# Kernel tuning notes

Measured on AMD Instinct MI355X. Metric: run time of the kernel, lower is better.

The kernel has to match this reference:

```python
import jax, jax.numpy as jnp
import numpy as np

NUM_ELEC = 128
TIME_STEPS = 128  # must equal NUM_ELEC for the original module's matmuls to be shape-consistent
NUM_VOXELS = 2052
HIDDEN = 64
DCT_DIM = 512
BATCH = 64
RHO = 0.5
TAU = 0.1
PLV_THRESH = 0.5


def dct_matrix(N, K):
    n = np.arange(N)[None, :]
    k = np.arange(K)[:, None]
    m = np.sqrt(2.0 / N) * np.cos(np.pi * (2 * n + 1) * k / (2 * N))
    m[0, :] = 1.0 / np.sqrt(N)
    return jnp.asarray(m, dtype=jnp.float32)


def setup_inputs() -> dict:
    ks = jax.random.split(jax.random.key(0), 12)
    H = HIDDEN
    return {
        "z": jax.random.normal(ks[0], (BATCH, NUM_ELEC, TIME_STEPS), dtype=jnp.float32),
        "lead_field": jax.random.normal(ks[1], (NUM_VOXELS, NUM_ELEC), dtype=jnp.float32),
        "gumbel_u": jax.random.uniform(ks[2], (NUM_ELEC, NUM_ELEC), dtype=jnp.float32, minval=1e-6, maxval=1.0 - 1e-6),
        "w_gae": jax.random.normal(ks[3], (NUM_ELEC, H), dtype=jnp.float32) / np.sqrt(NUM_ELEC),
        "b_gae": jnp.zeros((H,), dtype=jnp.float32),
        "w1": jax.random.normal(ks[4], (NUM_ELEC, H), dtype=jnp.float32) / np.sqrt(NUM_ELEC),
        "b1": jnp.zeros((H,), dtype=jnp.float32),
        "w2": jax.random.normal(ks[5], (H, H), dtype=jnp.float32) / np.sqrt(H),
        "b2": jnp.zeros((H,), dtype=jnp.float32),
        "w_ih": jax.random.normal(ks[6], (3 * H, H), dtype=jnp.float32) / np.sqrt(H),
        "w_hh": jax.random.normal(ks[7], (3 * H, H), dtype=jnp.float32) / np.sqrt(H),
        "b_ih": jnp.zeros((3 * H,), dtype=jnp.float32),
        "b_hh": jnp.zeros((3 * H,), dtype=jnp.float32),
    }


def _hilbert_phases(z):
    # FFT-based analytic signal along last axis (== scipy.signal.hilbert), then instantaneous phase
    T = z.shape[-1]
    idx = jnp.arange(T)
    hf = jnp.where(idx == 0, 1.0, jnp.where(idx < T // 2, 2.0, jnp.where(idx == T // 2, 1.0, 0.0)))
    analytic = jnp.fft.ifft(jnp.fft.fft(z, axis=-1) * hf, axis=-1)
    return jnp.angle(analytic)


def _forward(z, lead_field, gumbel_u, w_gae, b_gae, w1, b1, w2, b2, w_ih, w_hh, b_ih, b_hh):
    B, N, T = z.shape
    # ---- PLV adjacency: fused broadcast+reduction replacing the 128x128 python double loop ----
    phases = _hilbert_phases(z)                                  # [B,N,T]
    E = jnp.exp(1j * phases).astype(jnp.complex64)
    # plv[i,j] = |mean_{b,t} exp(i(phi_i - phi_j))| = |E_i . conj(E_j)| / (B*T)
    plv = jnp.abs(jnp.einsum('bit,bjt->ij', E, jnp.conj(E))) / (B * T)
    a = (plv >= PLV_THRESH).astype(jnp.float32)                  # [N,N]
    # ---- GAE: GCN encoder on batch-averaged signals + inner-product decoder ----
    x = jnp.mean(z, axis=0)                                      # [N,T] (T == N)
    hg = jax.nn.relu((a @ x) @ w_gae + b_gae)                    # [N,H]
    p = jax.nn.sigmoid(hg @ hg.T)                                # [N,N]
    # ---- Gumbel graph augmentation ----
    e = RHO * p + (1.0 - RHO) * a
    g = -jnp.log(-jnp.log(gumbel_u))
    a_aug = jax.nn.sigmoid((jnp.log(e) - jnp.log(1.0 - e) + g) / TAU)
    # ---- symmetric degree normalization ----
    d_inv_sqrt = jnp.sum(a_aug, axis=-1) ** -0.5
    a_norm = d_inv_sqrt[:, None] * a_aug * d_inv_sqrt[None, :]
    zT = jnp.swapaxes(z, 1, 2)                                   # [B,T,N]
    h = jax.nn.relu(jnp.matmul(a_norm, zT) @ w1 + b1)            # [B,N,H]
    h = jax.nn.relu(jnp.matmul(a_norm, h) @ w2 + b2)             # [B,N,H]
    h_seq = h.reshape(B * T, -1)                                 # [B*T,H]
    # ---- GRU over flattened (B*T) sequence (torch nn.GRU gate order r,z,n) ----
    Hd = w_hh.shape[1]
    def gru_step(hprev, xt):
        gi = xt @ w_ih.T + b_ih
        gh = hprev @ w_hh.T + b_hh
        ir, iz, inn = jnp.split(gi, 3)
        hr, hz, hn = jnp.split(gh, 3)
        r = jax.nn.sigmoid(ir + hr)
        zg = jax.nn.sigmoid(iz + hz)
        cand = jnp.tanh(inn + r * hn)
        hnew = (1.0 - zg) * cand + zg * hprev
        return hnew, hnew
    _, h_gru = jax.lax.scan(gru_step, jnp.zeros((Hd,), z.dtype), h_seq)
    del h_gru  # computed as in the original forward, but not part of the returned tuple
    # ---- lead-field projection + DCT low-pass reconstruction ----
    dct_m = dct_matrix(NUM_VOXELS, DCT_DIM)                      # [K,V]
    s = jnp.matmul(lead_field, zT)                               # [B,V,T]
    s_dct = jnp.matmul(dct_m, s)                                 # [B,K,T]
    s_low = s_dct[:, :DCT_DIM, :]                                # [B,K,T] (full, K == dct_dim)
    s_recon = jnp.matmul(dct_m.T, s_low)                         # [B,V,T]
    return s_low, s_recon, a_aug


def reference(z, lead_field, gumbel_u, w_gae, b_gae, w1, b1, w2, b2, w_ih, w_hh, b_ih, b_hh):
    return _forward(z, lead_field, gumbel_u, w_gae, b_gae, w1, b1, w2, b2, w_ih, w_hh, b_ih, b_hh)
```

## Files before the change

kernel.cpp:

```cpp
#include <hip/hip_runtime.h>

#define NV 2052
#define KD 512
#define RTOT 2564
#define KTOT 256
#define JTOT 8192

typedef __attribute__((ext_vector_type(8))) short short8v;
typedef __attribute__((ext_vector_type(4))) float f32x4;
typedef unsigned short ushort_t;

#define OFF_AF   0u
#define OFF_ABF  65536u
#define OFF_BBF  409600u
#define OFF_YBF  1458176u
#define OFF_PG   2506752u
#define OFF_PM1  6701056u
#define OFF_A    7749632u
#define OFF_X    7766016u
#define OFF_HG   7782400u

#define SREC_OFF 4194304u
#define AAUG_OFF 21004288u

#define GLOAD16(g, l) __builtin_amdgcn_global_load_lds( \
    (const __attribute__((address_space(1))) unsigned int*)(g), \
    (__attribute__((address_space(3))) unsigned int*)(l), 16, 0, 0)

__device__ __forceinline__ float dct_val(int k, int v) {
    if (k == 0) return 1.0f / sqrtf(2052.0f);
    int m = (2 * v + 1) * k;
    int r = m % 8208;
    float ang = (float)((double)r * (3.14159265358979323846 / 4104.0));
    return sqrtf(2.0f / 2052.0f) * cosf(ang);
}

__device__ __forceinline__ void bf16split(float x, ushort_t& hi, ushort_t& lo) {
    unsigned xb = __float_as_uint(x);
    hi = (ushort_t)(xb >> 16);
    float r = x - __uint_as_float((unsigned)hi << 16);
    lo = (ushort_t)(__float_as_uint(r) >> 16);
}

__device__ __forceinline__ ushort_t bf16rn(float x) {
    unsigned xb = __float_as_uint(x);
    return (ushort_t)((xb + 0x7fffu + ((xb >> 16) & 1u)) >> 16);
}

__global__ __launch_bounds__(256) void k_front(const float* __restrict__ LF, const float* __restrict__ z,
                                               float* __restrict__ Pm1,
                                               ushort_t* __restrict__ Ybf, ushort_t* __restrict__ Bbf) {
    __shared__ float sh[8][132];
    const int tid = threadIdx.x;
    const int bid = blockIdx.x;
    if (bid < 1024) {
        const int t = tid & 127;
        const int kk = tid >> 7;
        const int k0 = (bid & 63) * 8;
        const int vch = bid >> 6;
        const int v0 = vch * 128;
        const int nv = (vch == 15) ? 132 : 128;
        for (int p = tid; p < 1056; p += 256) {
            int rr = p / 132, cc = p - rr * 132;
            sh[rr][cc] = dct_val(k0 + rr, v0 + cc);
        }
        __syncthreads();
        const float* lf = LF + (size_t)v0 * 128 + t;
        float a0 = 0.f, a1 = 0.f, a2 = 0.f, a3 = 0.f;
        for (int vi = 0; vi + 2 <= nv; vi += 2) {
            float l0 = lf[vi * 128], l1 = lf[vi * 128 + 128];
            a0 += sh[kk + 0][vi] * l0; a1 += sh[kk + 2][vi] * l0;
            a2 += sh[kk + 4][vi] * l0; a3 += sh[kk + 6][vi] * l0;
            a0 += sh[kk + 0][vi + 1] * l1; a1 += sh[kk + 2][vi + 1] * l1;
            a2 += sh[kk + 4][vi + 1] * l1; a3 += sh[kk + 6][vi + 1] * l1;
        }
        float* P = Pm1 + (size_t)vch * 65536;
        P[(k0 + kk + 0) * 128 + t] = a0;
        P[(k0 + kk + 2) * 128 + t] = a1;
        P[(k0 + kk + 4) * 128 + t] = a2;
        P[(k0 + kk + 6) * 128 + t] = a3;
    } else {
        const int t = tid & 127;
        const int rr = tid >> 7;
        const int rid = (bid - 1024) * 2 + rr;
        const int b = rid >> 7, i = rid & 127;
        sh[rr][t] = z[(size_t)rid * 128 + t];
        if (tid < 128) {
            float hv = 0.f;
            if (t & 1) {
                float ang = 3.14159265358979323846f * (float)t * (1.0f / 128.0f);
                hv = (cosf(ang) / sinf(ang)) * (1.0f / 64.0f);
            }
            sh[2][t] = hv;
        }
        __syncthreads();
        float acc = 0.f;
        #pragma unroll 8
        for (int q = 0; q < 64; ++q) {
            int d = 2 * q + 1;
            acc += sh[2][d] * sh[rr][(t - d) & 127];
        }
        float zv = sh[rr][t];
        float inv = rsqrtf(zv * zv + acc * acc);
        Ybf[(size_t)i * JTOT + b * 128 + t] = bf16rn(zv * inv);
        Ybf[(size_t)(128 + i) * JTOT + b * 128 + t] = bf16rn(acc * inv);
        ushort_t hi = (ushort_t)(__float_as_uint(zv) >> 16);
        ushort_t* row = Bbf + (size_t)rid * KTOT;
        row[t] = hi; row[128 + t] = hi;
    }
}

__global__ __launch_bounds__(256) void k_m1red(const float* __restrict__ Pm1, float* __restrict__ AF,
                                               ushort_t* __restrict__ Abf) {
    int id = blockIdx.x * 256 + threadIdx.x;
    float s = 0.f;
    #pragma unroll
    for (int p = 0; p < 16; ++p) s += Pm1[p * 65536 + id];
    AF[id] = s;
    int rid = id >> 7, t = id & 127;
    ushort_t hi, lo; bf16split(s, hi, lo);
    ushort_t* row = Abf + (size_t)rid * KTOT;
    row[t] = hi; row[128 + t] = lo;
}

__global__ __launch_bounds__(256) void k_m2(const float* __restrict__ M1, ushort_t* __restrict__ Abf) {
    __shared__ float sd[2][128];
    const int tid = threadIdx.x;
    const int t = tid & 127;
    const int vv = tid >> 7;
    const int myv = blockIdx.x * 2 + vv;
    float a0 = 0.f, a1 = 0.f, a2 = 0.f, a3 = 0.f;
    for (int kc = 0; kc < KD; kc += 128) {
        __syncthreads();
        sd[vv][t] = dct_val(kc + t, myv);
        __syncthreads();
        const float* m1 = M1 + (size_t)kc * 128 + t;
        #pragma unroll 8
        for (int ki = 0; ki < 32; ++ki) {
            a0 += sd[vv][ki +  0] * m1[(ki +  0) * 128];
            a1 += sd[vv][ki + 32] * m1[(ki + 32) * 128];
            a2 += sd[vv][ki + 64] * m1[(ki + 64) * 128];
            a3 += sd[vv][ki + 96] * m1[(ki + 96) * 128];
        }
    }
    float s = (a0 + a1) + (a2 + a3);
    ushort_t hi, lo; bf16split(s, hi, lo);
    ushort_t* row = Abf + (size_t)(KD + myv) * KTOT;
    row[t] = hi; row[128 + t] = lo;
}

__global__ __launch_bounds__(256) void k_back(const ushort_t* __restrict__ Abf, const ushort_t* __restrict__ Bbf,
                                              const ushort_t* __restrict__ Ybf,
                                              float* __restrict__ out, float* __restrict__ Pg) {
    __shared__ float SMf[8704];
    ushort_t* Al = (ushort_t*)SMf;
    ushort_t* Bl = Al + 8192;
    const int tid = threadIdx.x;
    const int wave = tid >> 6;
    const int lane = tid & 63;
    const int wr = wave >> 1, wc = wave & 1;
    const int l15 = lane & 15;
    const int lhi = lane >> 4;
    const int bid = blockIdx.x;

    f32x4 acc[4][4];
    #pragma unroll
    for (int i = 0; i < 4; ++i)
        #pragma unroll
        for (int j = 0; j < 4; ++j)
            acc[i][j] = (f32x4){0.f, 0.f, 0.f, 0.f};

    if (bid < 1344) {
        const int j0 = (bid & 63) * 128;
        const int r0 = (bid >> 6) * 128;
        for (int kc = 0; kc < KTOT; kc += 64) {
            __syncthreads();
            #pragma unroll
            for (int i = 0; i < 4; ++i) {
                int elt = (wave * 4 + i) * 64 + lane;
                int m = elt >> 3;
                int sc = (elt & 7) ^ (m & 7);
                GLOAD16(Abf + (size_t)(r0 + m) * KTOT + kc + sc * 8, &Al[(wave * 4 + i) * 512]);
                GLOAD16(Bbf + (size_t)(j0 + m) * KTOT + kc + sc * 8, &Bl[(wave * 4 + i) * 512]);
            }
            asm volatile("s_waitcnt vmcnt(0)" ::: "memory");
            __syncthreads();
            #pragma unroll
            for (int kk = 0; kk < 2; ++kk) {
                short8v av[4], bv[4];
                #pragma unroll
                for (int mi = 0; mi < 4; ++mi) {
                    int m = wr * 64 + mi * 16 + l15;
                    int ch = (kk * 4 + lhi) ^ (m & 7);
                    av[mi] = *(const short8v*)&Al[m * 64 + ch * 8];
                }
                #pragma unroll
                for (int ni = 0; ni < 4; ++ni) {
                    int n = wc * 64 + ni * 16 + l15;
                    int ch = (kk * 4 + lhi) ^ (n & 7);
                    bv[ni] = *(const short8v*)&Bl[n * 64 + ch * 8];
                }
                #pragma unroll
                for (int mi = 0; mi < 4; ++mi)
                    #pragma unroll
                    for (int ni = 0; ni < 4; ++ni)
                        acc[mi][ni] = __builtin_amdgcn_mfma_f32_16x16x32_bf16(av[mi], bv[ni], acc[mi][ni], 0, 0, 0);
            }
        }
        const unsigned bb = (unsigned)(bid & 63);
        #pragma unroll
        for (int hhalf = 0; hhalf < 2; ++hhalf) {
            __syncthreads();
            if (wc == hhalf) {
                #pragma unroll
                for (int mi = 0; mi < 4; ++mi)
                    #pragma unroll
                    for (int ni = 0; ni < 4; ++ni)
                        #pragma unroll
                        for (int reg = 0; reg < 4; ++reg) {
                            int rl = wr * 64 + mi * 16 + lhi * 4 + reg;
                            int cl = ni * 16 + l15;
                            SMf[rl * 68 + cl] = acc[mi][ni][reg];
                        }
            }
            __syncthreads();
            int rl = tid >> 1;
            int cs = (tid & 1) * 32;
            int r = r0 + rl;
            if (r < RTOT) {
                unsigned base;
                if (r < KD) base = bb * 65536u + (unsigned)r * 128u;
                else        base = SREC_OFF + bb * 262656u + (unsigned)(r - KD) * 128u;
                base += hhalf * 64 + cs;
                const float* src = &SMf[rl * 68 + cs];
                float* dst = out + base;
                #pragma unroll
                for (int q = 0; q < 8; ++q)
                    *(float4*)(dst + q * 4) = *(const float4*)(src + q * 4);
            }
        }
    } else {
        const int g = bid - 1344;
        const int j0 = (g & 1) * 128;
        const int i0 = ((g >> 1) & 1) * 128;
        const int sk = g >> 2;
        const int kc0 = sk * 128;
        for (int kc = kc0; kc < kc0 + 128; kc += 64) {
            __syncthreads();
            #pragma unroll
            for (int i = 0; i < 4; ++i) {
                int elt = (wave * 4 + i) * 64 + lane;
                int m = elt >> 3;
                int sc = (elt & 7) ^ (m & 7);
                GLOAD16(Ybf + (size_t)(i0 + m) * JTOT + kc + sc * 8, &Al[(wave * 4 + i) * 512]);
                GLOAD16(Ybf + (size_t)(j0 + m) * JTOT + kc + sc * 8, &Bl[(wave * 4 + i) * 512]);
            }
            asm volatile("s_waitcnt vmcnt(0)" ::: "memory");
            __syncthreads();
            #pragma unroll
            for (int kk = 0; kk < 2; ++kk) {
                short8v av[4], bv[4];
                #pragma unroll
                for (int mi = 0; mi < 4; ++mi) {
                    int m = wr * 64 + mi * 16 + l15;
                    int ch = (kk * 4 + lhi) ^ (m & 7);
                    av[mi] = *(const short8v*)&Al[m * 64 + ch * 8];
                }
                #pragma unroll
                for (int ni = 0; ni < 4; ++ni) {
                    int n = wc * 64 + ni * 16 + l15;
                    int ch = (kk * 4 + lhi) ^ (n & 7);
                    bv[ni] = *(const short8v*)&Bl[n * 64 + ch * 8];
                }
                #pragma unroll
                for (int mi = 0; mi < 4; ++mi)
                    #pragma unroll
                    for (int ni = 0; ni < 4; ++ni)
                        acc[mi][ni] = __builtin_amdgcn_mfma_f32_16x16x32_bf16(av[mi], bv[ni], acc[mi][ni], 0, 0, 0);
            }
        }
        const int q = ((g >> 1) & 1) * 2 + (g & 1);
        float* P = Pg + (size_t)(sk * 4 + q) * 16384;
        #pragma unroll
        for (int mi = 0; mi < 4; ++mi)
            #pragma unroll
            for (int reg = 0; reg < 4; ++reg) {
                int rl = wr * 64 + mi * 16 + lhi * 4 + reg;
                #pragma unroll
                for (int ni = 0; ni < 4; ++ni) {
                    int cl = wc * 64 + ni * 16 + l15;
                    P[rl * 128 + cl] = acc[mi][ni][reg];
                }
            }
    }
}

__global__ __launch_bounds__(256) void k_plvx(const float* __restrict__ Pg, const float* __restrict__ z,
                                              float* __restrict__ A, float* __restrict__ X) {
    int id = blockIdx.x * 256 + threadIdx.x;
    float R = 0.f, I = 0.f;
    #pragma unroll 8
    for (int sk = 0; sk < 64; ++sk) {
        const float* P = Pg + (size_t)sk * 65536 + id;
        R += P[0] + P[3 * 16384];
        I += P[2 * 16384] - P[1 * 16384];
    }
    float plv = sqrtf(R * R + I * I) * (1.0f / 8192.0f);
    A[id] = (plv >= 0.5f) ? 1.0f : 0.0f;
    float s = 0.f;
    for (int b = 0; b < 64; ++b) s += z[(size_t)b * 16384 + id];
    X[id] = s * (1.0f / 64.0f);
}

__global__ __launch_bounds__(256) void k_axhg(const float* __restrict__ A, const float* __restrict__ X,
                                              const float* __restrict__ Wg, const float* __restrict__ bg,
                                              float* __restrict__ HG) {
    __shared__ float sAX[2][128];
    const int tid = threadIdx.x;
    const int t = tid & 127;
    const int ii = tid >> 7;
    const int i = blockIdx.x * 2 + ii;
    float s = 0.f;
    const float* arow = A + (size_t)i * 128;
    #pragma unroll 4
    for (int j = 0; j < 128; ++j) s += arow[j] * X[j * 128 + t];
    sAX[ii][t] = s;
    __syncthreads();
    if (tid < 128) {
        int i2 = tid >> 6;
        int h = tid & 63;
        float v = bg[h];
        #pragma unroll 4
        for (int t2 = 0; t2 < 128; ++t2) v += sAX[i2][t2] * Wg[t2 * 64 + h];
        HG[(size_t)(blockIdx.x * 2 + i2) * 64 + h] = fmaxf(v, 0.f);
    }
}

__global__ __launch_bounds__(256) void k_aaug(const float* __restrict__ HG, const float* __restrict__ A,
                                              const float* __restrict__ U, float* __restrict__ out) {
    int id = blockIdx.x * 256 + threadIdx.x;
    int i = id >> 7, j = id & 127;
    float dot = 0.f;
    #pragma unroll 8
    for (int h = 0; h < 64; ++h) dot += HG[i * 64 + h] * HG[j * 64 + h];
    float p = 1.f / (1.f + expf(-dot));
    float e = 0.5f * p + 0.5f * A[id];
    float gmb = -logf(-logf(U[id]));
    float arg = (logf(e) - logf(1.f - e) + gmb) * 10.0f;
    out[AAUG_OFF + id] = 1.f / (1.f + expf(-arg));
}

extern "C" void kernel_launch(void* const* d_in, const int* in_sizes, int n_in,
                              void* d_out, int out_size, void* d_ws, size_t ws_size,
                              hipStream_t stream) {
    const float* z  = (const float*)d_in[0];
    const float* LF = (const float*)d_in[1];
    const float* U  = (const float*)d_in[2];
    const float* Wg = (const float*)d_in[3];
    const float* bg = (const float*)d_in[4];
    float* out = (float*)d_out;
    float* W = (float*)d_ws;

    float* AF  = W + OFF_AF;
    ushort_t* Abf = (ushort_t*)(W + OFF_ABF);
    ushort_t* Bbf = (ushort_t*)(W + OFF_BBF);
    ushort_t* Ybf = (ushort_t*)(W + OFF_YBF);
    float* Pg  = W + OFF_PG;
    float* Pm1 = W + OFF_PM1;
    float* A   = W + OFF_A;
    float* X   = W + OFF_X;
    float* HG  = W + OFF_HG;

    k_front<<<5120, 256, 0, stream>>>(LF, z, Pm1, Ybf, Bbf);
    k_m1red<<<256, 256, 0, stream>>>(Pm1, AF, Abf);
    k_m2   <<<1026, 256, 0, stream>>>(AF, Abf);
    k_back <<<1600, 256, 0, stream>>>(Abf, Bbf, Ybf, out, Pg);
    k_plvx <<<64, 256, 0, stream>>>(Pg, z, A, X);
    k_axhg <<<64, 256, 0, stream>>>(A, X, Wg, bg, HG);
    k_aaug <<<64, 256, 0, stream>>>(HG, A, U, out);
}
```

Before: 119.3 us.

## Double-buffer LDS tiles in k_back to overlap global loads with MFMA

```diff
diff --git a/kernel.cpp b/kernel.cpp
--- a/kernel.cpp
+++ b/kernel.cpp
@@ -152,9 +152,7 @@
 __global__ __launch_bounds__(256) void k_back(const ushort_t* __restrict__ Abf, const ushort_t* __restrict__ Bbf,
                                               const ushort_t* __restrict__ Ybf,
                                               float* __restrict__ out, float* __restrict__ Pg) {
-    __shared__ float SMf[8704];
-    ushort_t* Al = (ushort_t*)SMf;
-    ushort_t* Bl = Al + 8192;
+    __shared__ ushort_t SM[2][16384];
     const int tid = threadIdx.x;
     const int wave = tid >> 6;
     const int lane = tid & 63;
@@ -173,18 +171,30 @@
     if (bid < 1344) {
         const int j0 = (bid & 63) * 128;
         const int r0 = (bid >> 6) * 128;
-        for (int kc = 0; kc < KTOT; kc += 64) {
-            __syncthreads();
+        auto stageG = [&](int buf, int kc) {
             #pragma unroll
             for (int i = 0; i < 4; ++i) {
                 int elt = (wave * 4 + i) * 64 + lane;
                 int m = elt >> 3;
                 int sc = (elt & 7) ^ (m & 7);
-                GLOAD16(Abf + (size_t)(r0 + m) * KTOT + kc + sc * 8, &Al[(wave * 4 + i) * 512]);
-                GLOAD16(Bbf + (size_t)(j0 + m) * KTOT + kc + sc * 8, &Bl[(wave * 4 + i) * 512]);
-            }
-            asm volatile("s_waitcnt vmcnt(0)" ::: "memory");
-            __syncthreads();
+                GLOAD16(Abf + (size_t)(r0 + m) * KTOT + kc + sc * 8, &SM[buf][(wave * 4 + i) * 512]);
+                GLOAD16(Bbf + (size_t)(j0 + m) * KTOT + kc + sc * 8, &SM[buf][8192 + (wave * 4 + i) * 512]);
+            }
+        };
+        stageG(0, 0);
+        #pragma unroll
+        for (int t = 0; t < 4; ++t) {
+            __builtin_amdgcn_s_barrier();
+            if (t < 3) {
+                stageG((t + 1) & 1, (t + 1) * 64);
+                asm volatile("s_waitcnt vmcnt(8)" ::: "memory");
+            } else {
+                asm volatile("s_waitcnt vmcnt(0)" ::: "memory");
+            }
+            __builtin_amdgcn_s_barrier();
+            __builtin_amdgcn_sched_barrier(0);
+            const ushort_t* Al = &SM[t & 1][0];
+            const ushort_t* Bl = &SM[t & 1][8192];
             #pragma unroll
             for (int kk = 0; kk < 2; ++kk) {
                 short8v av[4], bv[4];
@@ -207,6 +217,7 @@
                         acc[mi][ni] = __builtin_amdgcn_mfma_f32_16x16x32_bf16(av[mi], bv[ni], acc[mi][ni], 0, 0, 0);
             }
         }
+        float* SMf = (float*)&SM[0][0];
         const unsigned bb = (unsigned)(bid & 63);
         #pragma unroll
         for (int hhalf = 0; hhalf < 2; ++hhalf) {
@@ -245,18 +256,30 @@
         const int i0 = ((g >> 1) & 1) * 128;
         const int sk = g >> 2;
         const int kc0 = sk * 128;
-        for (int kc = kc0; kc < kc0 + 128; kc += 64) {
-            __syncthreads();
+        auto stageY = [&](int buf, int kc) {
             #pragma unroll
             for (int i = 0; i < 4; ++i) {
                 int elt = (wave * 4 + i) * 64 + lane;
                 int m = elt >> 3;
                 int sc = (elt & 7) ^ (m & 7);
-                GLOAD16(Ybf + (size_t)(i0 + m) * JTOT + kc + sc * 8, &Al[(wave * 4 + i) * 512]);
-                GLOAD16(Ybf + (size_t)(j0 + m) * JTOT + kc + sc * 8, &Bl[(wave * 4 + i) * 512]);
-            }
-            asm volatile("s_waitcnt vmcnt(0)" ::: "memory");
-            __syncthreads();
+                GLOAD16(Ybf + (size_t)(i0 + m) * JTOT + kc + sc * 8, &SM[buf][(wave * 4 + i) * 512]);
+                GLOAD16(Ybf + (size_t)(j0 + m) * JTOT + kc + sc * 8, &SM[buf][8192 + (wave * 4 + i) * 512]);
+            }
+        };
+        stageY(0, kc0);
+        #pragma unroll
+        for (int t = 0; t < 2; ++t) {
+            __builtin_amdgcn_s_barrier();
+            if (t < 1) {
+                stageY(1, kc0 + 64);
+                asm volatile("s_waitcnt vmcnt(8)" ::: "memory");
+            } else {
+                asm volatile("s_waitcnt vmcnt(0)" ::: "memory");
+            }
+            __builtin_amdgcn_s_barrier();
+            __builtin_amdgcn_sched_barrier(0);
+            const ushort_t* Al = &SM[t][0];
+            const ushort_t* Bl = &SM[t][8192];
             #pragma unroll
             for (int kk = 0; kk < 2; ++kk) {
                 short8v av[4], bv[4];
```

After: 120.5 us. No clear change (+1.0%).

## Move X mean and X·Wg off the tail and fuse GAE into aaug

Applied to the files above, without the earlier changes.

```diff
diff --git a/kernel.cpp b/kernel.cpp
--- a/kernel.cpp
+++ b/kernel.cpp
@@ -18,7 +18,7 @@
 #define OFF_PM1  6701056u
 #define OFF_A    7749632u
 #define OFF_X    7766016u
-#define OFF_HG   7782400u
+#define OFF_XW   7782400u
 
 #define SREC_OFF 4194304u
 #define AAUG_OFF 21004288u
@@ -110,22 +110,56 @@
     }
 }
 
-__global__ __launch_bounds__(256) void k_m1red(const float* __restrict__ Pm1, float* __restrict__ AF,
-                                               ushort_t* __restrict__ Abf) {
-    int id = blockIdx.x * 256 + threadIdx.x;
-    float s = 0.f;
-    #pragma unroll
-    for (int p = 0; p < 16; ++p) s += Pm1[p * 65536 + id];
-    AF[id] = s;
-    int rid = id >> 7, t = id & 127;
-    ushort_t hi, lo; bf16split(s, hi, lo);
-    ushort_t* row = Abf + (size_t)rid * KTOT;
-    row[t] = hi; row[128 + t] = lo;
-}
-
-__global__ __launch_bounds__(256) void k_m2(const float* __restrict__ M1, ushort_t* __restrict__ Abf) {
+__global__ __launch_bounds__(256) void k_m1red(const float* __restrict__ Pm1, const float* __restrict__ z,
+                                               float* __restrict__ AF, ushort_t* __restrict__ Abf,
+                                               float* __restrict__ X) {
+    const int bid = blockIdx.x;
+    if (bid < 256) {
+        int id = bid * 256 + threadIdx.x;
+        float s = 0.f;
+        #pragma unroll
+        for (int p = 0; p < 16; ++p) s += Pm1[p * 65536 + id];
+        AF[id] = s;
+        int rid = id >> 7, t = id & 127;
+        ushort_t hi, lo; bf16split(s, hi, lo);
+        ushort_t* row = Abf + (size_t)rid * KTOT;
+        row[t] = hi; row[128 + t] = lo;
+    } else {
+        int id = (bid - 256) * 256 + threadIdx.x;
+        float s0 = 0.f, s1 = 0.f, s2 = 0.f, s3 = 0.f;
+        #pragma unroll 4
+        for (int b = 0; b < 64; b += 4) {
+            s0 += z[(size_t)(b + 0) * 16384 + id];
+            s1 += z[(size_t)(b + 1) * 16384 + id];
+            s2 += z[(size_t)(b + 2) * 16384 + id];
+            s3 += z[(size_t)(b + 3) * 16384 + id];
+        }
+        X[id] = ((s0 + s1) + (s2 + s3)) * (1.0f / 64.0f);
+    }
+}
+
+__global__ __launch_bounds__(256) void k_m2(const float* __restrict__ M1, ushort_t* __restrict__ Abf,
+                                            const float* __restrict__ X, const float* __restrict__ Wg,
+                                            float* __restrict__ XW) {
     __shared__ float sd[2][128];
     const int tid = threadIdx.x;
+    if (blockIdx.x == 1026) {
+        const int e = tid >> 1;
+        const int h0 = (tid & 1) * 32;
+        float acc[32];
+        #pragma unroll
+        for (int h = 0; h < 32; ++h) acc[h] = 0.f;
+        const float* xrow = X + (size_t)e * 128;
+        for (int t = 0; t < 128; ++t) {
+            float xv = xrow[t];
+            const float* wrow = Wg + (size_t)t * 64 + h0;
+            #pragma unroll
+            for (int h = 0; h < 32; ++h) acc[h] += xv * wrow[h];
+        }
+        #pragma unroll
+        for (int h = 0; h < 32; ++h) XW[(size_t)e * 64 + h0 + h] = acc[h];
+        return;
+    }
     const int t = tid & 127;
     const int vv = tid >> 7;
     const int myv = blockIdx.x * 2 + vv;
@@ -295,8 +329,7 @@
     }
 }
 
-__global__ __launch_bounds__(256) void k_plvx(const float* __restrict__ Pg, const float* __restrict__ z,
-                                              float* __restrict__ A, float* __restrict__ X) {
+__global__ __launch_bounds__(256) void k_plvx(const float* __restrict__ Pg, float* __restrict__ A) {
     int id = blockIdx.x * 256 + threadIdx.x;
     float R = 0.f, I = 0.f;
     #pragma unroll 8
@@ -307,42 +340,38 @@
     }
     float plv = sqrtf(R * R + I * I) * (1.0f / 8192.0f);
     A[id] = (plv >= 0.5f) ? 1.0f : 0.0f;
-    float s = 0.f;
-    for (int b = 0; b < 64; ++b) s += z[(size_t)b * 16384 + id];
-    X[id] = s * (1.0f / 64.0f);
-}
-
-__global__ __launch_bounds__(256) void k_axhg(const float* __restrict__ A, const float* __restrict__ X,
-                                              const float* __restrict__ Wg, const float* __restrict__ bg,
-                                              float* __restrict__ HG) {
-    __shared__ float sAX[2][128];
+}
+
+__global__ __launch_bounds__(256) void k_aaugf(const float* __restrict__ A, const float* __restrict__ XW,
+                                               const float* __restrict__ bg, const float* __restrict__ U,
+                                               float* __restrict__ out) {
+    __shared__ float sXW[128][64];
+    __shared__ float sHGT[64][128];
     const int tid = threadIdx.x;
-    const int t = tid & 127;
-    const int ii = tid >> 7;
-    const int i = blockIdx.x * 2 + ii;
-    float s = 0.f;
-    const float* arow = A + (size_t)i * 128;
-    #pragma unroll 4
-    for (int j = 0; j < 128; ++j) s += arow[j] * X[j * 128 + t];
-    sAX[ii][t] = s;
+    for (int p = tid; p < 8192; p += 256) sXW[p >> 6][p & 63] = XW[p];
     __syncthreads();
-    if (tid < 128) {
-        int i2 = tid >> 6;
-        int h = tid & 63;
-        float v = bg[h];
-        #pragma unroll 4
-        for (int t2 = 0; t2 < 128; ++t2) v += sAX[i2][t2] * Wg[t2 * 64 + h];
-        HG[(size_t)(blockIdx.x * 2 + i2) * 64 + h] = fmaxf(v, 0.f);
-    }
-}
-
-__global__ __launch_bounds__(256) void k_aaug(const float* __restrict__ HG, const float* __restrict__ A,
-                                              const float* __restrict__ U, float* __restrict__ out) {
-    int id = blockIdx.x * 256 + threadIdx.x;
-    int i = id >> 7, j = id & 127;
+    {
+        const int r = tid & 127;
+        const int half = tid >> 7;
+        const float* arow = A + (size_t)r * 128;
+        float hacc[32];
+        #pragma unroll
+        for (int h = 0; h < 32; ++h) hacc[h] = 0.f;
+        for (int j = 0; j < 128; ++j) {
+            float av = arow[j];
+            #pragma unroll
+            for (int h = 0; h < 32; ++h) hacc[h] += av * sXW[j][half * 32 + h];
+        }
+        #pragma unroll
+        for (int h = 0; h < 32; ++h)
+            sHGT[half * 32 + h][r] = fmaxf(hacc[h] + bg[half * 32 + h], 0.f);
+    }
+    __syncthreads();
+    const int id = blockIdx.x * 256 + tid;
+    const int i = id >> 7, j = id & 127;
     float dot = 0.f;
     #pragma unroll 8
-    for (int h = 0; h < 64; ++h) dot += HG[i * 64 + h] * HG[j * 64 + h];
+    for (int h = 0; h < 64; ++h) dot += sHGT[h][i] * sHGT[h][j];
     float p = 1.f / (1.f + expf(-dot));
     float e = 0.5f * p + 0.5f * A[id];
     float gmb = -logf(-logf(U[id]));
@@ -369,13 +398,12 @@
     float* Pm1 = W + OFF_PM1;
     float* A   = W + OFF_A;
     float* X   = W + OFF_X;
-    float* HG  = W + OFF_HG;
+    float* XW  = W + OFF_XW;
 
     k_front<<<5120, 256, 0, stream>>>(LF, z, Pm1, Ybf, Bbf);
-    k_m1red<<<256, 256, 0, stream>>>(Pm1, AF, Abf);
-    k_m2   <<<1026, 256, 0, stream>>>(AF, Abf);
+    k_m1red<<<320, 256, 0, stream>>>(Pm1, z, AF, Abf, X);
+    k_m2   <<<1027, 256, 0, stream>>>(AF, Abf, X, Wg, XW);
     k_back <<<1600, 256, 0, stream>>>(Abf, Bbf, Ybf, out, Pg);
-    k_plvx <<<64, 256, 0, stream>>>(Pg, z, A, X);
-    k_axhg <<<64, 256, 0, stream>>>(A, X, Wg, bg, HG);
-    k_aaug <<<64, 256, 0, stream>>>(HG, A, U, out);
-}
+    k_plvx <<<64, 256, 0, stream>>>(Pg, A);
+    k_aaugf<<<64, 256, 0, stream>>>(A, XW, bg, U, out);
+}
```

Measured after the change: 164.0 us. 37.5% more time.
